# Kernel optimization log

Hardware: AMD Instinct MI355X
Metric: run time of the kernel (lower is better)

Reference implementation:

```python
import jax, jax.numpy as jnp
import numpy as np

DIM = 1024
N_HEADS = 16
HEAD_DIM = DIM // N_HEADS
LORA_DIM = 16
B, T = 4, 1024


def _rope(x):
    # x: [B, H, T, D] with D even; rotate first/second halves (torch impl style)
    D = x.shape[-1]
    half = D // 2
    theta = 1.0 / (10000.0 ** (jnp.arange(0, D, 2, dtype=jnp.float32) / D))  # [D/2]
    pos = jnp.arange(x.shape[-2], dtype=jnp.float32)                         # [T]
    pt = pos[:, None] * theta[None, :]                                       # [T, D/2]
    sin, cos = jnp.sin(pt), jnp.cos(pt)
    xr, xi = x[..., :half], x[..., half:]
    return jnp.concatenate([xr * cos - xi * sin, xr * sin + xi * cos], axis=-1)


def setup_inputs() -> dict:
    key = jax.random.key(0)
    ks = jax.random.split(key, 16)
    def n(k, shape, std=0.02):
        return jax.random.normal(k, shape, jnp.float32) * std
    return {
        "x": jax.random.normal(ks[0], (B, T, DIM), jnp.float32),
        "q_w": n(ks[1], (DIM, DIM)),
        "k_w": n(ks[2], (DIM, DIM)),
        "v_w": n(ks[3], (DIM, DIM)),
        "q_a": n(ks[4], (LORA_DIM, DIM), 0.001),
        "q_b": n(ks[5], (DIM, LORA_DIM), 0.001),
        "q_l": jax.random.normal(ks[6], (DIM,), jnp.float32),
        "k_a": n(ks[7], (LORA_DIM, DIM), 0.001),
        "k_b": n(ks[8], (DIM, LORA_DIM), 0.001),
        "k_l": jax.random.normal(ks[9], (DIM,), jnp.float32),
        "v_a": n(ks[10], (LORA_DIM, DIM), 0.001),
        "v_b": n(ks[11], (DIM, LORA_DIM), 0.001),
        "v_l": jax.random.normal(ks[12], (DIM,), jnp.float32),
        "proj_w": n(ks[13], (DIM, DIM)),
        "proj_b": n(ks[14], (DIM,)),
    }


def reference(x, q_w, k_w, v_w, q_a, q_b, q_l, k_a, k_b, k_l,
              v_a, v_b, v_l, proj_w, proj_b):
    Bb, Tt, C = x.shape
    # token shift: xx[t] = x[t-1], xx[0] = 0 (ZeroPad2d((0,0,1,-1)))
    xx = jnp.pad(x, ((0, 0), (1, 0), (0, 0)))[:, :Tt]
    xxx = xx - x

    def lora(a, b, lam):
        return lam + jnp.tanh(x @ a.T) @ b.T  # [B,T,C]

    q = (x + xxx * lora(q_a, q_b, q_l)) @ q_w.T
    k = (x + xxx * lora(k_a, k_b, k_l)) @ k_w.T
    v = (x + xxx * lora(v_a, v_b, v_l)) @ v_w.T

    def split_heads(t):
        return t.reshape(Bb, Tt, N_HEADS, HEAD_DIM).transpose(0, 2, 1, 3)  # [B,H,T,D]

    q = _rope(split_heads(q))
    k = _rope(split_heads(k))
    v = split_heads(v)

    scale = 1.0 / np.sqrt(HEAD_DIM).astype(np.float32)
    scores = jnp.einsum('bhqd,bhkd->bhqk', q, k) * scale
    causal = jnp.tril(jnp.ones((Tt, Tt), dtype=bool))
    scores = jnp.where(causal, scores, jnp.float32(-1e30))
    att = jax.nn.softmax(scores, axis=-1)
    out = jnp.einsum('bhqk,bhkd->bhqd', att, v)
    out = out.transpose(0, 2, 1, 3).reshape(Bb, Tt, C)
    return out @ proj_w.T + proj_b
```

## Files before the change

### kernel.cpp

```cpp
#include <hip/hip_runtime.h>
#include <hip/hip_bf16.h>

typedef __hip_bfloat16 bf16;
typedef __attribute__((ext_vector_type(8))) short bf16x8;
typedef __attribute__((ext_vector_type(4))) float f32x4;

typedef const __attribute__((address_space(1))) unsigned int* gp_t;
typedef __attribute__((address_space(3))) unsigned int* lp_t;

__device__ __forceinline__ bf16 tobf(float f) { return __float2bfloat16(f); }
__device__ __forceinline__ float tof(bf16 h) { return __bfloat162float(h); }

__device__ __forceinline__ short bfbits(float f) {
    bf16 h = __float2bfloat16(f);
    return *reinterpret_cast<short*>(&h);
}
__device__ __forceinline__ bf16x8 pack8(float4 a, float4 b) {
    bf16x8 r;
    r[0] = bfbits(a.x); r[1] = bfbits(a.y); r[2] = bfbits(a.z); r[3] = bfbits(a.w);
    r[4] = bfbits(b.x); r[5] = bfbits(b.y); r[6] = bfbits(b.z); r[7] = bfbits(b.w);
    return r;
}

__device__ __forceinline__ void gload_lds16(const void* g, void* l) {
    __builtin_amdgcn_global_load_lds((gp_t)g, (lp_t)l, 16, 0, 0);
}

__global__ __launch_bounds__(256) void lora_gate_fused(
    const float* x,
    const float* qa, const float* ka, const float* va,
    const float* qbw, const float* ql,
    const float* kbw, const float* kl,
    const float* vbw, const float* vl,
    const float* qw, const float* kw, const float* vw, const float* pw,
    bf16* wdst,
    bf16* xqo, bf16* xko, bf16* xvo) {
    const int XS = 1028;
    int row0 = blockIdx.x * 8;
    int t0 = row0 & 1023;
    int tid = threadIdx.x;
    int wave = tid >> 6, lane = tid & 63;
    int quad = lane >> 4, l16 = lane & 15;

    __shared__ float sx[9 * 1028];
    __shared__ float sT[8 * 48];

    {
        int prow = (row0 == 0) ? 0 : row0 - 1;
        for (int i = 0; i < 9; ++i) {
            int grow = (i == 0) ? prow : row0 + i - 1;
            gload_lds16(x + (size_t)grow * 1024 + wave * 256 + lane * 4,
                        &sx[i * XS + wave * 256]);
        }
    }
    {
        int m = blockIdx.x >> 7;
        const float* src = m == 0 ? qw : (m == 1 ? kw : (m == 2 ? vw : pw));
        bf16* dst = wdst + (size_t)m * (1u << 20);
        int off = (blockIdx.x & 127) * 8192;
#pragma unroll
        for (int u = 0; u < 8; ++u) {
            int i = off + u * 1024 + tid * 4;
            float4 f = *(const float4*)(src + i);
            ushort4 o4;
            o4.x = (unsigned short)bfbits(f.x);
            o4.y = (unsigned short)bfbits(f.y);
            o4.z = (unsigned short)bfbits(f.z);
            o4.w = (unsigned short)bfbits(f.w);
            *(ushort4*)&dst[i] = o4;
        }
    }
    __syncthreads();

    if (wave < 3) {
        const float* am = wave == 0 ? qa : (wave == 1 ? ka : va);
        int xr = (l16 < 8) ? l16 : 7;
        f32x4 acc = (f32x4){0.f, 0.f, 0.f, 0.f};
#pragma unroll 4
        for (int k0 = 0; k0 < 1024; k0 += 32) {
            const float* xs = &sx[(1 + xr) * XS + k0 + quad * 8];
            bf16x8 af = pack8(*(const float4*)xs, *(const float4*)(xs + 4));
            const float* as = am + (size_t)l16 * 1024 + k0 + quad * 8;
            bf16x8 bf_ = pack8(*(const float4*)as, *(const float4*)(as + 4));
            acc = __builtin_amdgcn_mfma_f32_16x16x32_bf16(af, bf_, acc, 0, 0, 0);
        }
#pragma unroll
        for (int r = 0; r < 4; ++r) {
            int row = quad * 4 + r;
            if (row < 8) sT[row * 48 + wave * 16 + l16] = tanhf(acc[r]);
        }
    }
    __syncthreads();

#pragma unroll
    for (int u = 0; u < 4; ++u) {
        int d = tid + u * 256;
        float qbv[16], kbv[16], vbv[16];
#pragma unroll
        for (int p = 0; p < 4; ++p) {
            *(float4*)&qbv[p * 4] = *(const float4*)(qbw + (size_t)d * 16 + p * 4);
            *(float4*)&kbv[p * 4] = *(const float4*)(kbw + (size_t)d * 16 + p * 4);
            *(float4*)&vbv[p * 4] = *(const float4*)(vbw + (size_t)d * 16 + p * 4);
        }
        float qlv = ql[d], klv = kl[d], vlv = vl[d];
        float xp = (t0 == 0) ? 0.f : sx[0 * XS + d];
        for (int rr = 0; rr < 8; ++rr) {
            float xc = sx[(rr + 1) * XS + d];
            float dx = xp - xc;
            float gq = qlv, gk = klv, gv = vlv;
#pragma unroll
            for (int j = 0; j < 16; ++j) {
                gq += sT[rr * 48 + j] * qbv[j];
                gk += sT[rr * 48 + 16 + j] * kbv[j];
                gv += sT[rr * 48 + 32 + j] * vbv[j];
            }
            size_t o = (size_t)(row0 + rr) * 1024 + d;
            xqo[o] = tobf(xc + dx * gq);
            xko[o] = tobf(xc + dx * gk);
            xvo[o] = tobf(xc + dx * gv);
            xp = xc;
        }
    }
}

__global__ __launch_bounds__(256) void gemm128(
    const bf16* A0, const bf16* A1, const bf16* A2,
    const bf16* W0, const bf16* W1, const bf16* W2,
    bf16* C0, bf16* C1, bf16* C2,
    const float* bias, float* outF, int proj, int zcnt) {
    const int K = 1024;
    int ppx = (zcnt * 32) >> 3;
    int xcd = blockIdx.x & 7;
    int j = blockIdx.x >> 3;
    int pair = xcd * ppx + (j >> 3);
    int n0 = (j & 7) * 128;
    int bz = pair >> 5;
    int m0 = (pair & 31) * 128;

    const bf16* A = bz == 0 ? A0 : (bz == 1 ? A1 : A2);
    const bf16* W = bz == 0 ? W0 : (bz == 1 ? W1 : W2);
    bf16* C = bz == 0 ? C0 : (bz == 1 ? C1 : C2);

    __shared__ alignas(16) bf16 sA[64 * 64];
    __shared__ alignas(16) bf16 sB[64 * 64];

    int wave = threadIdx.x >> 6, lane = threadIdx.x & 63;
    int quad = lane >> 4, l16 = lane & 15;

    f32x4 acc[4][4];
#pragma unroll
    for (int i = 0; i < 4; i++)
#pragma unroll
        for (int j2 = 0; j2 < 4; j2++) acc[i][j2] = (f32x4){0.f, 0.f, 0.f, 0.f};

    int Rb0 = wave * 16 + (lane >> 3);
    int s0 = lane & 7;

    auto stage = [&](int k0) {
#pragma unroll
        for (int p = 0; p < 2; p++) {
            int R = Rb0 + p * 8;
            int cs = s0 ^ (R & 7);
            int mr = 2 * R + (cs >> 2);
            int kc = (cs & 3) * 8;
            gload_lds16(A + (size_t)(m0 + mr) * K + k0 + kc, &sA[(wave * 16 + p * 8) * 64]);
            gload_lds16(W + (size_t)(n0 + mr) * K + k0 + kc, &sB[(wave * 16 + p * 8) * 64]);
        }
    };

    int mw = (wave >> 1) * 64, nw = (wave & 1) * 64;
    int slot = (((l16 & 1) << 2) | quad) ^ ((l16 >> 1) & 7);
    int abase = ((mw >> 1) + (l16 >> 1)) * 64 + slot * 8;
    int bbase = ((nw >> 1) + (l16 >> 1)) * 64 + slot * 8;

    for (int it = 0; it < 32; ++it) {
        __syncthreads();
        stage(it * 32);
        __syncthreads();
        bf16x8 af[4], bfr[4];
#pragma unroll
        for (int f = 0; f < 4; f++) {
            af[f] = *(const bf16x8*)&sA[abase + f * 512];
            bfr[f] = *(const bf16x8*)&sB[bbase + f * 512];
        }
#pragma unroll
        for (int i = 0; i < 4; i++)
#pragma unroll
            for (int j2 = 0; j2 < 4; j2++)
                acc[i][j2] = __builtin_amdgcn_mfma_f32_16x16x32_bf16(af[i], bfr[j2], acc[i][j2], 0, 0, 0);
    }

    if (proj) {
#pragma unroll
        for (int i = 0; i < 4; i++) {
            int mrow = m0 + mw + i * 16 + quad * 4;
#pragma unroll
            for (int j2 = 0; j2 < 4; j2++) {
                int col = n0 + nw + j2 * 16 + l16;
                float bv = bias[col];
#pragma unroll
                for (int r = 0; r < 4; r++)
                    outF[(size_t)(mrow + r) * 1024 + col] = acc[i][j2][r] + bv;
            }
        }
    } else if (bz < 2) {
        float sc = (bz == 0) ? 0.125f : 1.0f;
        int tb = ((m0 + mw) & 1023) + quad * 4;
#pragma unroll
        for (int j2 = 0; j2 < 2; j2++) {
            int d = j2 * 16 + l16;
            float theta = __expf(-(float)d * (9.210340371976184f / 32.0f));
            float s1, c1, s16, c16, st, ct;
            sincosf(theta, &s1, &c1);
            sincosf(16.0f * theta, &s16, &c16);
            sincosf((float)tb * theta, &st, &ct);
            int col = n0 + nw + j2 * 16 + l16;
#pragma unroll
            for (int i = 0; i < 4; i++) {
                int mrow = m0 + mw + i * 16 + quad * 4;
                float c = ct, s = st;
#pragma unroll
                for (int r = 0; r < 4; r++) {
                    float xr = acc[i][j2][r], xi = acc[i][j2 + 2][r];
                    C[(size_t)(mrow + r) * 1024 + col] = tobf((xr * c - xi * s) * sc);
                    C[(size_t)(mrow + r) * 1024 + col + 32] = tobf((xr * s + xi * c) * sc);
                    float cn = c * c1 - s * s1;
                    s = s * c1 + c * s1;
                    c = cn;
                }
                float cn = ct * c16 - st * s16;
                st = st * c16 + ct * s16;
                ct = cn;
            }
        }
    } else {
#pragma unroll
        for (int i = 0; i < 4; i++) {
            int mrow = m0 + mw + i * 16 + quad * 4;
#pragma unroll
            for (int j2 = 0; j2 < 4; j2++) {
                int col = n0 + nw + j2 * 16 + l16;
#pragma unroll
                for (int r = 0; r < 4; r++)
                    C[(size_t)(mrow + r) * 1024 + col] = tobf(acc[i][j2][r]);
            }
        }
    }
}

__global__ __launch_bounds__(256) void v_transpose(const bf16* v, bf16* Vt) {
    int bh = blockIdx.x, tblk = blockIdx.y;
    int b = bh >> 4, h = bh & 15;
    int t0 = tblk * 64;
    int tid = threadIdx.x;

    __shared__ bf16 sv[64 * 65];
    {
        int r = tid >> 2;
        int c0 = (tid & 3) * 16;
        size_t g = ((size_t)(b * 1024 + t0 + r)) * 1024 + h * 64 + c0;
#pragma unroll
        for (int u = 0; u < 16; u++) sv[(c0 + u) * 65 + r] = v[g + u];
    }
    __syncthreads();
    {
        int d = tid >> 2;
        int tc = (tid & 3) * 16;
        size_t g = ((size_t)(bh * 64 + d)) * 1024 + t0 + tc;
#pragma unroll
        for (int u = 0; u < 16; u++) Vt[g + u] = sv[d * 65 + tc + u];
    }
}

__global__ __launch_bounds__(256) void attention(const bf16* Qm, const bf16* Km,
                                                 const bf16* Vt, bf16* attn) {
    int gid = blockIdx.x;
    int qblk = 15 - (gid >> 6);
    int bh = (((gid >> 3) & 7) << 3) | (gid & 7);
    int b = bh >> 4, h = bh & 15;
    int wave = threadIdx.x >> 6, lane = threadIdx.x & 63;
    int quad = lane >> 4, l16 = lane & 15;
    int m7 = l16 & 7;

    const bf16* Qb = Qm + (size_t)b * 1024 * 1024 + h * 64;
    const bf16* Kb = Km + (size_t)b * 1024 * 1024 + h * 64;
    const bf16* Vb = Vt + (size_t)bh * 64 * 1024;

    __shared__ alignas(16) bf16 sK[2][64 * 64];
    __shared__ alignas(16) bf16 sV[2][64 * 64];
    __shared__ alignas(16) bf16 sP[4][16 * 64];

    int srow = lane >> 3;
    int scol = ((lane & 7) ^ srow) * 8;

    auto stage = [&](int kt, int bufi) {
#pragma unroll
        for (int p = 0; p < 2; p++) {
            int rbase = p * 32 + wave * 8;
            gload_lds16(Kb + (size_t)(kt * 64 + rbase + srow) * 1024 + scol, &sK[bufi][rbase * 64]);
            gload_lds16(Vb + (size_t)(rbase + srow) * 1024 + kt * 64 + scol, &sV[bufi][rbase * 64]);
        }
    };

    int qrow0 = qblk * 64 + wave * 16;
    bf16x8 aq0 = *(const bf16x8*)&Qb[(size_t)(qrow0 + l16) * 1024 + quad * 8];
    bf16x8 aq1 = *(const bf16x8*)&Qb[(size_t)(qrow0 + l16) * 1024 + quad * 8 + 32];

    f32x4 o[4];
#pragma unroll
    for (int nt = 0; nt < 4; nt++) o[nt] = (f32x4){0.f, 0.f, 0.f, 0.f};
    float lpart[4] = {0.f, 0.f, 0.f, 0.f};

    stage(0, 0);

    int buf = 0;
    for (int kt = 0; kt <= qblk; ++kt, buf ^= 1) {
        __syncthreads();
        if (kt < qblk) stage(kt + 1, buf ^ 1);

        f32x4 S[4];
#pragma unroll
        for (int j = 0; j < 4; j++) {
            int row = j * 16 + l16;
            bf16x8 bk0 = *(const bf16x8*)&sK[buf][row * 64 + ((quad ^ m7) * 8)];
            bf16x8 bk1 = *(const bf16x8*)&sK[buf][row * 64 + (((quad + 4) ^ m7) * 8)];
            f32x4 z = __builtin_amdgcn_mfma_f32_16x16x32_bf16(aq0, bk0, (f32x4){0.f, 0.f, 0.f, 0.f}, 0, 0, 0);
            S[j] = __builtin_amdgcn_mfma_f32_16x16x32_bf16(aq1, bk1, z, 0, 0, 0);
        }
        if (kt == qblk) {
#pragma unroll
            for (int j = 0; j < 4; j++) {
                int key = kt * 64 + j * 16 + l16;
#pragma unroll
                for (int r = 0; r < 4; r++) {
                    int qr = qrow0 + quad * 4 + r;
                    if (key > qr) S[j][r] = -3.0e38f;
                }
            }
        }
#pragma unroll
        for (int j = 0; j < 4; j++)
#pragma unroll
            for (int r = 0; r < 4; r++) {
                float p = __expf(S[j][r]);
                S[j][r] = p;
                lpart[r] += p;
            }

#pragma unroll
        for (int j = 0; j < 4; j++) {
            int c = j * 2 + (l16 >> 3);
#pragma unroll
            for (int r = 0; r < 4; r++) {
                int prow = quad * 4 + r;
                sP[wave][prow * 64 + ((c ^ (prow & 7)) * 8) + m7] = tobf(S[j][r]);
            }
        }
        asm volatile("s_waitcnt lgkmcnt(0)" ::: "memory");
        bf16x8 ap0 = *(const bf16x8*)&sP[wave][l16 * 64 + ((quad ^ m7) * 8)];
        bf16x8 ap1 = *(const bf16x8*)&sP[wave][l16 * 64 + (((quad + 4) ^ m7) * 8)];
#pragma unroll
        for (int nt = 0; nt < 4; nt++) {
            int row = nt * 16 + l16;
            bf16x8 bv0 = *(const bf16x8*)&sV[buf][row * 64 + ((quad ^ m7) * 8)];
            bf16x8 bv1 = *(const bf16x8*)&sV[buf][row * 64 + (((quad + 4) ^ m7) * 8)];
            o[nt] = __builtin_amdgcn_mfma_f32_16x16x32_bf16(ap0, bv0, o[nt], 0, 0, 0);
            o[nt] = __builtin_amdgcn_mfma_f32_16x16x32_bf16(ap1, bv1, o[nt], 0, 0, 0);
        }
    }

    float invl[4];
#pragma unroll
    for (int r = 0; r < 4; r++) {
        float v = lpart[r];
        v += __shfl_xor(v, 1);
        v += __shfl_xor(v, 2);
        v += __shfl_xor(v, 4);
        v += __shfl_xor(v, 8);
        invl[r] = 1.0f / v;
    }
#pragma unroll
    for (int nt = 0; nt < 4; nt++)
#pragma unroll
        for (int r = 0; r < 4; r++) {
            int t = qrow0 + quad * 4 + r;
            int col = h * 64 + nt * 16 + l16;
            attn[(size_t)(b * 1024 + t) * 1024 + col] = tobf(o[nt][r] * invl[r]);
        }
}

extern "C" void kernel_launch(void* const* d_in, const int* in_sizes, int n_in,
                              void* d_out, int out_size, void* d_ws, size_t ws_size,
                              hipStream_t stream) {
    const float* x = (const float*)d_in[0];
    const float* qw = (const float*)d_in[1];
    const float* kw = (const float*)d_in[2];
    const float* vw = (const float*)d_in[3];
    const float* qa = (const float*)d_in[4];
    const float* qb = (const float*)d_in[5];
    const float* ql = (const float*)d_in[6];
    const float* ka = (const float*)d_in[7];
    const float* kb = (const float*)d_in[8];
    const float* kl = (const float*)d_in[9];
    const float* va = (const float*)d_in[10];
    const float* vb = (const float*)d_in[11];
    const float* vl = (const float*)d_in[12];
    const float* pw = (const float*)d_in[13];
    const float* pb = (const float*)d_in[14];
    float* out = (float*)d_out;

    char* ws = (char*)d_ws;
    const size_t MB = 1024 * 1024;
    bf16* wqb = (bf16*)ws;
    bf16* wkb = wqb + 1048576;
    bf16* wvb = wkb + 1048576;
    bf16* wpb = wvb + 1048576;
    bf16* xqb = (bf16*)(ws + 8 * MB);
    bf16* xkb = xqb + 4194304;
    bf16* xvb = xkb + 4194304;
    bf16* qm = (bf16*)(ws + 32 * MB);
    bf16* km = qm + 4194304;
    bf16* vm = km + 4194304;
    bf16* Vt = xvb;
    bf16* attn = xqb;

    lora_gate_fused<<<512, 256, 0, stream>>>(x, qa, ka, va, qb, ql, kb, kl, vb, vl,
                                             qw, kw, vw, pw, wqb,
                                             xqb, xkb, xvb);
    gemm128<<<768, 256, 0, stream>>>(xqb, xkb, xvb, wqb, wkb, wvb, qm, km, vm,
                                     nullptr, nullptr, 0, 3);
    v_transpose<<<dim3(64, 16), 256, 0, stream>>>(vm, Vt);
    attention<<<1024, 256, 0, stream>>>(qm, km, Vt, attn);
    gemm128<<<256, 256, 0, stream>>>(attn, nullptr, nullptr, wpb, nullptr, nullptr,
                                     nullptr, nullptr, nullptr, pb, out, 1, 1);
}
```

Baseline: 212.0 us.

## Fuse V transpose into QKV GEMM epilogue and split LoRA-A reduction across waves

The QKV GEMM now writes V directly in a transposed [h*64+d][b*1024+t] layout with 4-element vector stores, so the separate v_transpose kernel and its launch and memory round trip are removed. Attention's V staging reads use the new stride to match. The LoRA down-projection in the gate kernel now has all four waves each compute a K-quarter for all three adapters, combining the partial sums through shared memory before tanh, so the fourth wave is no longer idle. The transposed epilogue stores are strided by 4096 elements per column, which may be less coalesced than the original row-major writes.

```diff
diff --git a/kernel.cpp b/kernel.cpp
--- a/kernel.cpp
+++ b/kernel.cpp
@@ -43,6 +43,7 @@
     int quad = lane >> 4, l16 = lane & 15;
 
     __shared__ float sx[9 * 1028];
+    __shared__ float spT[3][4][8][17];
     __shared__ float sT[8 * 48];
 
     {
@@ -72,23 +73,40 @@
     }
     __syncthreads();
 
-    if (wave < 3) {
-        const float* am = wave == 0 ? qa : (wave == 1 ? ka : va);
+    {
         int xr = (l16 < 8) ? l16 : 7;
-        f32x4 acc = (f32x4){0.f, 0.f, 0.f, 0.f};
-#pragma unroll 4
-        for (int k0 = 0; k0 < 1024; k0 += 32) {
+        f32x4 acc[3];
+#pragma unroll
+        for (int m = 0; m < 3; m++) acc[m] = (f32x4){0.f, 0.f, 0.f, 0.f};
+        int kb = wave * 256;
+#pragma unroll
+        for (int kk = 0; kk < 256; kk += 32) {
+            int k0 = kb + kk;
             const float* xs = &sx[(1 + xr) * XS + k0 + quad * 8];
             bf16x8 af = pack8(*(const float4*)xs, *(const float4*)(xs + 4));
-            const float* as = am + (size_t)l16 * 1024 + k0 + quad * 8;
-            bf16x8 bf_ = pack8(*(const float4*)as, *(const float4*)(as + 4));
-            acc = __builtin_amdgcn_mfma_f32_16x16x32_bf16(af, bf_, acc, 0, 0, 0);
-        }
-#pragma unroll
-        for (int r = 0; r < 4; ++r) {
-            int row = quad * 4 + r;
-            if (row < 8) sT[row * 48 + wave * 16 + l16] = tanhf(acc[r]);
-        }
+#pragma unroll
+            for (int m = 0; m < 3; m++) {
+                const float* am = m == 0 ? qa : (m == 1 ? ka : va);
+                const float* as = am + (size_t)l16 * 1024 + k0 + quad * 8;
+                bf16x8 bf_ = pack8(*(const float4*)as, *(const float4*)(as + 4));
+                acc[m] = __builtin_amdgcn_mfma_f32_16x16x32_bf16(af, bf_, acc[m], 0, 0, 0);
+            }
+        }
+#pragma unroll
+        for (int m = 0; m < 3; m++)
+#pragma unroll
+            for (int r = 0; r < 4; r++) {
+                int row = quad * 4 + r;
+                if (row < 8) spT[m][wave][row][l16] = acc[m][r];
+            }
+    }
+    __syncthreads();
+    if (tid < 384) {
+        int m = tid >> 7, idx = tid & 127;
+        int row = idx >> 4, col = idx & 15;
+        float v = spT[m][0][row][col] + spT[m][1][row][col]
+                + spT[m][2][row][col] + spT[m][3][row][col];
+        sT[row * 48 + m * 16 + col] = tanhf(v);
     }
     __syncthreads();
 
@@ -240,35 +258,14 @@
 #pragma unroll
             for (int j2 = 0; j2 < 4; j2++) {
                 int col = n0 + nw + j2 * 16 + l16;
-#pragma unroll
-                for (int r = 0; r < 4; r++)
-                    C[(size_t)(mrow + r) * 1024 + col] = tobf(acc[i][j2][r]);
-            }
-        }
-    }
-}
-
-__global__ __launch_bounds__(256) void v_transpose(const bf16* v, bf16* Vt) {
-    int bh = blockIdx.x, tblk = blockIdx.y;
-    int b = bh >> 4, h = bh & 15;
-    int t0 = tblk * 64;
-    int tid = threadIdx.x;
-
-    __shared__ bf16 sv[64 * 65];
-    {
-        int r = tid >> 2;
-        int c0 = (tid & 3) * 16;
-        size_t g = ((size_t)(b * 1024 + t0 + r)) * 1024 + h * 64 + c0;
-#pragma unroll
-        for (int u = 0; u < 16; u++) sv[(c0 + u) * 65 + r] = v[g + u];
-    }
-    __syncthreads();
-    {
-        int d = tid >> 2;
-        int tc = (tid & 3) * 16;
-        size_t g = ((size_t)(bh * 64 + d)) * 1024 + t0 + tc;
-#pragma unroll
-        for (int u = 0; u < 16; u++) Vt[g + u] = sv[d * 65 + tc + u];
+                ushort4 o4;
+                o4.x = (unsigned short)bfbits(acc[i][j2][0]);
+                o4.y = (unsigned short)bfbits(acc[i][j2][1]);
+                o4.z = (unsigned short)bfbits(acc[i][j2][2]);
+                o4.w = (unsigned short)bfbits(acc[i][j2][3]);
+                *(ushort4*)&C[(size_t)col * 4096 + mrow] = o4;
+            }
+        }
     }
 }
 
@@ -284,7 +281,7 @@
 
     const bf16* Qb = Qm + (size_t)b * 1024 * 1024 + h * 64;
     const bf16* Kb = Km + (size_t)b * 1024 * 1024 + h * 64;
-    const bf16* Vb = Vt + (size_t)bh * 64 * 1024;
+    const bf16* Vb = Vt + (size_t)(h * 64) * 4096 + b * 1024;
 
     __shared__ alignas(16) bf16 sK[2][64 * 64];
     __shared__ alignas(16) bf16 sV[2][64 * 64];
@@ -298,7 +295,7 @@
         for (int p = 0; p < 2; p++) {
             int rbase = p * 32 + wave * 8;
             gload_lds16(Kb + (size_t)(kt * 64 + rbase + srow) * 1024 + scol, &sK[bufi][rbase * 64]);
-            gload_lds16(Vb + (size_t)(rbase + srow) * 1024 + kt * 64 + scol, &sV[bufi][rbase * 64]);
+            gload_lds16(Vb + (size_t)(rbase + srow) * 4096 + kt * 64 + scol, &sV[bufi][rbase * 64]);
         }
     };
 
@@ -420,16 +417,14 @@
     bf16* xvb = xkb + 4194304;
     bf16* qm = (bf16*)(ws + 32 * MB);
     bf16* km = qm + 4194304;
-    bf16* vm = km + 4194304;
-    bf16* Vt = xvb;
+    bf16* Vt = km + 4194304;
     bf16* attn = xqb;
 
     lora_gate_fused<<<512, 256, 0, stream>>>(x, qa, ka, va, qb, ql, kb, kl, vb, vl,
                                              qw, kw, vw, pw, wqb,
                                              xqb, xkb, xvb);
-    gemm128<<<768, 256, 0, stream>>>(xqb, xkb, xvb, wqb, wkb, wvb, qm, km, vm,
+    gemm128<<<768, 256, 0, stream>>>(xqb, xkb, xvb, wqb, wkb, wvb, qm, km, Vt,
                                      nullptr, nullptr, 0, 3);
-    v_transpose<<<dim3(64, 16), 256, 0, stream>>>(vm, Vt);
     attention<<<1024, 256, 0, stream>>>(qm, km, Vt, attn);
     gemm128<<<256, 256, 0, stream>>>(attn, nullptr, nullptr, wpb, nullptr, nullptr,
                                      nullptr, nullptr, nullptr, pb, out, 1, 1);
```

Result: faster. 204.5 us (-3.5%).
